# Kernel tuning notes

Hardware: AMD Instinct MI355X
Metric: run time of the kernel (lower is better)

The kernel has to match this reference:

```python
import jax, jax.numpy as jnp
import numpy as np

IMAGE_W = 256
IMAGE_H = 256
SIGMA = 0.2
EPS = 1e-07


def _gauss_filter(g, size, psize, pad):
    """g: [B,N] center coords in pixels. Returns [B,N,size,psize]."""
    # grid coords over padded canvas: value i - pad at row i (matches np.indices - pad)
    coords = jnp.arange(size + 2 * pad, dtype=jnp.float32) - pad          # [size+2pad]
    offs = jnp.arange(1, psize + 1, dtype=jnp.float32) - psize / 2 - 0.5  # [psize]
    mu = g[:, :, None] + offs[None, None, :]                              # [B,N,psize]
    F = jnp.exp(-(coords[None, None, :, None] - mu[:, :, None, :]) ** 2 / (2 * SIGMA ** 2))
    F = F / (F.sum(axis=2, keepdims=True) + EPS)
    return F[:, :, pad:size + pad]                                        # [B,N,size,psize]


def setup_inputs() -> dict:
    key = jax.random.key(0)
    k1, k2 = jax.random.split(key)
    brushes = jax.random.uniform(k1, (32, 64, 2), dtype=jnp.float32)
    patches = jax.random.normal(k2, (32, 64, 3, 16, 16), dtype=jnp.float32)
    return {"brushes": brushes, "patches": patches}


def reference(brushes, patches):
    B, N, C, ph, pw = patches.shape
    pad = ph // 2  # pad='half_patch'
    gx = brushes[:, :, 0] * IMAGE_W  # [B,N]
    gy = brushes[:, :, 1] * IMAGE_H
    Fx = _gauss_filter(gx, IMAGE_W, pw, pad)  # [B,N,w,pw]
    Fy = _gauss_filter(gy, IMAGE_H, ph, pad)  # [B,N,h,ph]
    # contract over pw: [B,N,C,w,ph]
    t = jnp.einsum('bnwq,bncpq->bncwp', Fx, patches)
    # contract over ph: [B,N,C,w,h]
    out = jnp.einsum('bncwp,bnhp->bncwh', t, Fy)
    out = out.mean(axis=1)            # [B,C,w,h]
    out = jnp.swapaxes(out, 2, 3)     # [B,C,h,w]
    return out
```

## Files before the change

### kernel.cpp

```cpp
#include <hip/hip_runtime.h>
#include <hip/hip_bf16.h>


#define E25 1.3887944e-11f

__global__ __launch_bounds__(256) void brush_tile32(
        const float* __restrict__ brushes,
        const float* __restrict__ patches,
        float* __restrict__ out)
{
    const int b    = blockIdx.z;
    const int tx   = blockIdx.x << 5;
    const int ty   = blockIdx.y << 5;
    const int tid  = threadIdx.x;
    const int lane = tid & 63;
    const int qi   = tid & 15;
    const int pi   = tid >> 4;

    __shared__ float4 T4[2 * 32 * 21];

    for (int i = tid; i < 320; i += 256) {
        const int buf = i / 160, r = i % 160;
        T4[buf * 672 + (r / 5) * 21 + 16 + (r % 5)] = make_float4(0, 0, 0, 0);
    }

    const float2 g0 = ((const float2*)brushes)[(b << 6) + lane];
    const float bx = g0.x * 256.0f, by = g0.y * 256.0f;
    const bool hit =
        (bx >= (float)tx - 9.5f) & (bx <= (float)tx + 40.5f) &
        (by >= (float)ty - 9.5f) & (by <= (float)ty + 40.5f);
    unsigned long long mask = __ballot(hit);

    float acc[2][2][3];
#pragma unroll
    for (int a = 0; a < 2; ++a)
#pragma unroll
        for (int h2 = 0; h2 < 2; ++h2)
            acc[a][h2][0] = acc[a][h2][1] = acc[a][h2][2] = 0.0f;

    int it = 0;
    while (mask) {
        const int n = __builtin_ctzll(mask);
        mask &= mask - 1;
        const float gx = __shfl(bx, n, 64);
        const float gy = __shfl(by, n, 64);
        const int buf = (it & 1) * 672; ++it;

        const float* pb = patches + (size_t)((b << 6) + n) * 768;
        const float r0 = pb[tid];
        const float r1 = pb[tid + 256];
        const float r2 = pb[tid + 512];

        float invz;
        {
            const int k = lane & 31;
            const float g  = (k >> 4) ? gy : gx;
            const float mu = g + (float)(k & 15) - 7.5f;
            const float fl = floorf(mu);
            float Z = 0.0f;
#pragma unroll
            for (int d = -1; d <= 2; ++d) {
                const float c = fl + (float)d;
                if (c >= -8.0f && c <= 263.0f) {
                    const float u = c - mu;
                    Z += __expf(-12.5f * u * u);
                }
            }
            invz = 1.0f / (Z + 1e-7f);
        }
        const float zx  = __shfl(invz, qi, 64);
        const float zyp = __shfl(invz, 16 + pi, 64);
        const float v0 = r0 * zx, v1 = r1 * zx, v2 = r2 * zx;

        const bool doA = (gx <= (float)tx + 24.5f);
        const bool doB = (gx >= (float)tx + 6.5f);

        float4 sA = make_float4(0, 0, 0, 0), sB = sA;
#pragma unroll
        for (int half = 0; half < 2; ++half) {
            const bool go = half ? doB : doA;
            if (!go) continue;
            const float ax = (float)(tx + (half << 4) + qi) - gx + 7.5f;
            const bool okx = (ax >= -2.5f) & (ax <= 17.5f);
            int qlo = (int)ceilf(ax - 2.0f);
            qlo = qlo < 0 ? 0 : (qlo > 15 ? 15 : qlo);
            float d0 = ax - (float)qlo;
            d0 = fminf(fmaxf(d0, -3.0f), 3.0f);
            float wgt = okx ? __expf(-12.5f * d0 * d0) : 0.0f;
            float u   = __expf(25.0f * d0 - 12.5f);
            const int base = ((pi & 3) << 4) + qlo;
            float4 s = make_float4(0, 0, 0, 0);
#pragma unroll
            for (int j = 0; j < 5; ++j) {
                const float a0 = __shfl(v0, base + j, 64);
                const float a1 = __shfl(v1, base + j, 64);
                const float a2 = __shfl(v2, base + j, 64);
                const float wj = (qlo + j < 16) ? wgt : 0.0f;
                s.x += wj * a0; s.y += wj * a1; s.z += wj * a2;
                wgt *= u; u *= E25;
            }
            s.x *= zyp; s.y *= zyp; s.z *= zyp;
            if (half) sB = s; else sA = s;
        }
        T4[buf + qi * 21 + pi]        = sA;
        T4[buf + (qi + 16) * 21 + pi] = sB;
        __syncthreads();

#pragma unroll
        for (int h2 = 0; h2 < 2; ++h2) {
            const float ay = (float)(ty + (h2 << 4) + pi) - gy + 7.5f;
            if (ay < -2.5f || ay > 17.5f) continue;
            int plo = (int)ceilf(ay - 2.0f);
            plo = plo < 0 ? 0 : (plo > 15 ? 15 : plo);
            const float d0 = ay - (float)plo;
            float wy[5];
            float wgt = __expf(-12.5f * d0 * d0);
            float u   = __expf(25.0f * d0 - 12.5f);
#pragma unroll
            for (int j = 0; j < 5; ++j) { wy[j] = wgt; wgt *= u; u *= E25; }
#pragma unroll
            for (int a = 0; a < 2; ++a) {
                if (!(a ? doB : doA)) continue;
                const float4* row = &T4[buf + (qi + (a << 4)) * 21 + plo];
                float s0 = 0.0f, s1 = 0.0f, s2 = 0.0f;
#pragma unroll
                for (int j = 0; j < 5; ++j) {
                    const float4 v = row[j];
                    s0 += wy[j] * v.x; s1 += wy[j] * v.y; s2 += wy[j] * v.z;
                }
                acc[a][h2][0] += s0; acc[a][h2][1] += s1; acc[a][h2][2] += s2;
            }
        }
    }

    const float sc = 1.0f / 64.0f;
#pragma unroll
    for (int a = 0; a < 2; ++a)
#pragma unroll
        for (int h2 = 0; h2 < 2; ++h2) {
            const int w = tx + (a << 4) + qi;
            const int h = ty + (h2 << 4) + pi;
            float* ob = out + (((size_t)(b * 3)) << 16) + (h << 8) + w;
            ob[0]       = acc[a][h2][0] * sc;
            ob[1 << 16] = acc[a][h2][1] * sc;
            ob[2 << 16] = acc[a][h2][2] * sc;
        }
}

extern "C" void kernel_launch(void* const* d_in, const int* in_sizes, int n_in,
                              void* d_out, int out_size, void* d_ws, size_t ws_size,
                              hipStream_t stream) {
    const float* brushes = (const float*)d_in[0];
    const float* patches = (const float*)d_in[1];
    float* out = (float*)d_out;
    brush_tile32<<<dim3(8, 8, 32), dim3(256), 0, stream>>>(brushes, patches, out);
}
```

Measured before the change: 80.64 us.

## Switch to one-wavefront blocks covering 16x16 output tiles

Replaces the 256-thread 32x32 tile kernel with a 64-thread kernel where one wavefront handles a 16x16 tile. Each lane processes four output rows and shuffles across four register groups. The smaller tile tightens the brush-overlap test so fewer brushes are visited per tile, and a single wave drops the cross-wave barrier cost and the double buffer. In exchange, patches are reloaded by more blocks and each lane does more shuffles.

```diff
diff --git a/kernel.cpp b/kernel.cpp
--- a/kernel.cpp
+++ b/kernel.cpp
@@ -4,58 +4,53 @@
 
 #define E25 1.3887944e-11f
 
-__global__ __launch_bounds__(256) void brush_tile32(
+__global__ __launch_bounds__(64) void brush_wave(
         const float* __restrict__ brushes,
         const float* __restrict__ patches,
         float* __restrict__ out)
 {
     const int b    = blockIdx.z;
-    const int tx   = blockIdx.x << 5;
-    const int ty   = blockIdx.y << 5;
-    const int tid  = threadIdx.x;
-    const int lane = tid & 63;
-    const int qi   = tid & 15;
-    const int pi   = tid >> 4;
+    const int tx   = blockIdx.x << 4;
+    const int ty   = blockIdx.y << 4;
+    const int lane = threadIdx.x;
+    const int qi   = lane & 15;
+    const int pi   = lane >> 4;
 
-    __shared__ float4 T4[2 * 32 * 21];
+    __shared__ float4 T4[16 * 21];
 
-    for (int i = tid; i < 320; i += 256) {
-        const int buf = i / 160, r = i % 160;
-        T4[buf * 672 + (r / 5) * 21 + 16 + (r % 5)] = make_float4(0, 0, 0, 0);
-    }
+    for (int i = lane; i < 80; i += 64)
+        T4[(i / 5) * 21 + 16 + (i % 5)] = make_float4(0, 0, 0, 0);
 
     const float2 g0 = ((const float2*)brushes)[(b << 6) + lane];
     const float bx = g0.x * 256.0f, by = g0.y * 256.0f;
     const bool hit =
-        (bx >= (float)tx - 9.5f) & (bx <= (float)tx + 40.5f) &
-        (by >= (float)ty - 9.5f) & (by <= (float)ty + 40.5f);
+        (bx >= (float)tx - 9.5f) & (bx <= (float)tx + 24.5f) &
+        (by >= (float)ty - 9.5f) & (by <= (float)ty + 24.5f);
     unsigned long long mask = __ballot(hit);
 
-    float acc[2][2][3];
+    float acc[4][3];
 #pragma unroll
-    for (int a = 0; a < 2; ++a)
-#pragma unroll
-        for (int h2 = 0; h2 < 2; ++h2)
-            acc[a][h2][0] = acc[a][h2][1] = acc[a][h2][2] = 0.0f;
+    for (int k = 0; k < 4; ++k) acc[k][0] = acc[k][1] = acc[k][2] = 0.0f;
 
-    int it = 0;
     while (mask) {
         const int n = __builtin_ctzll(mask);
         mask &= mask - 1;
         const float gx = __shfl(bx, n, 64);
         const float gy = __shfl(by, n, 64);
-        const int buf = (it & 1) * 672; ++it;
 
         const float* pb = patches + (size_t)((b << 6) + n) * 768;
-        const float r0 = pb[tid];
-        const float r1 = pb[tid + 256];
-        const float r2 = pb[tid + 512];
+        float r[3][4];
+#pragma unroll
+        for (int c = 0; c < 3; ++c)
+#pragma unroll
+            for (int k = 0; k < 4; ++k)
+                r[c][k] = pb[c * 256 + k * 64 + lane];
 
         float invz;
         {
-            const int k = lane & 31;
-            const float g  = (k >> 4) ? gy : gx;
-            const float mu = g + (float)(k & 15) - 7.5f;
+            const int k2 = lane & 31;
+            const float g  = (k2 >> 4) ? gy : gx;
+            const float mu = g + (float)(k2 & 15) - 7.5f;
             const float fl = floorf(mu);
             float Z = 0.0f;
 #pragma unroll
@@ -68,83 +63,75 @@
             }
             invz = 1.0f / (Z + 1e-7f);
         }
-        const float zx  = __shfl(invz, qi, 64);
-        const float zyp = __shfl(invz, 16 + pi, 64);
-        const float v0 = r0 * zx, v1 = r1 * zx, v2 = r2 * zx;
+        const float zx = __shfl(invz, qi, 64);
+        float zy[4];
+#pragma unroll
+        for (int k = 0; k < 4; ++k)
+            zy[k] = __shfl(invz, 16 + pi + 4 * k, 64);
 
-        const bool doA = (gx <= (float)tx + 24.5f);
-        const bool doB = (gx >= (float)tx + 6.5f);
+#pragma unroll
+        for (int c = 0; c < 3; ++c)
+#pragma unroll
+            for (int k = 0; k < 4; ++k)
+                r[c][k] *= zx;
 
-        float4 sA = make_float4(0, 0, 0, 0), sB = sA;
-#pragma unroll
-        for (int half = 0; half < 2; ++half) {
-            const bool go = half ? doB : doA;
-            if (!go) continue;
-            const float ax = (float)(tx + (half << 4) + qi) - gx + 7.5f;
-            const bool okx = (ax >= -2.5f) & (ax <= 17.5f);
+        {
+            const float ax  = (float)(tx + qi) - gx + 7.5f;
+            const bool  okx = (ax >= -2.5f) & (ax <= 17.5f);
             int qlo = (int)ceilf(ax - 2.0f);
             qlo = qlo < 0 ? 0 : (qlo > 15 ? 15 : qlo);
             float d0 = ax - (float)qlo;
             d0 = fminf(fmaxf(d0, -3.0f), 3.0f);
             float wgt = okx ? __expf(-12.5f * d0 * d0) : 0.0f;
             float u   = __expf(25.0f * d0 - 12.5f);
-            const int base = ((pi & 3) << 4) + qlo;
-            float4 s = make_float4(0, 0, 0, 0);
+            float s0[4] = {0, 0, 0, 0}, s1[4] = {0, 0, 0, 0}, s2[4] = {0, 0, 0, 0};
 #pragma unroll
             for (int j = 0; j < 5; ++j) {
-                const float a0 = __shfl(v0, base + j, 64);
-                const float a1 = __shfl(v1, base + j, 64);
-                const float a2 = __shfl(v2, base + j, 64);
-                const float wj = (qlo + j < 16) ? wgt : 0.0f;
-                s.x += wj * a0; s.y += wj * a1; s.z += wj * a2;
+                const float wj   = (qlo + j < 16) ? wgt : 0.0f;
+                const int   srcl = (pi << 4) + qlo + j;
+#pragma unroll
+                for (int k = 0; k < 4; ++k) {
+                    s0[k] += wj * __shfl(r[0][k], srcl, 64);
+                    s1[k] += wj * __shfl(r[1][k], srcl, 64);
+                    s2[k] += wj * __shfl(r[2][k], srcl, 64);
+                }
                 wgt *= u; u *= E25;
             }
-            s.x *= zyp; s.y *= zyp; s.z *= zyp;
-            if (half) sB = s; else sA = s;
+#pragma unroll
+            for (int k = 0; k < 4; ++k)
+                T4[qi * 21 + pi + 4 * k] =
+                    make_float4(s0[k] * zy[k], s1[k] * zy[k], s2[k] * zy[k], 0.0f);
         }
-        T4[buf + qi * 21 + pi]        = sA;
-        T4[buf + (qi + 16) * 21 + pi] = sB;
         __syncthreads();
 
 #pragma unroll
-        for (int h2 = 0; h2 < 2; ++h2) {
-            const float ay = (float)(ty + (h2 << 4) + pi) - gy + 7.5f;
+        for (int k = 0; k < 4; ++k) {
+            const float ay = (float)(ty + pi + 4 * k) - gy + 7.5f;
             if (ay < -2.5f || ay > 17.5f) continue;
             int plo = (int)ceilf(ay - 2.0f);
             plo = plo < 0 ? 0 : (plo > 15 ? 15 : plo);
             const float d0 = ay - (float)plo;
-            float wy[5];
             float wgt = __expf(-12.5f * d0 * d0);
             float u   = __expf(25.0f * d0 - 12.5f);
+            const float4* row = &T4[qi * 21 + plo];
 #pragma unroll
-            for (int j = 0; j < 5; ++j) { wy[j] = wgt; wgt *= u; u *= E25; }
-#pragma unroll
-            for (int a = 0; a < 2; ++a) {
-                if (!(a ? doB : doA)) continue;
-                const float4* row = &T4[buf + (qi + (a << 4)) * 21 + plo];
-                float s0 = 0.0f, s1 = 0.0f, s2 = 0.0f;
-#pragma unroll
-                for (int j = 0; j < 5; ++j) {
-                    const float4 v = row[j];
-                    s0 += wy[j] * v.x; s1 += wy[j] * v.y; s2 += wy[j] * v.z;
-                }
-                acc[a][h2][0] += s0; acc[a][h2][1] += s1; acc[a][h2][2] += s2;
+            for (int j = 0; j < 5; ++j) {
+                const float4 v = row[j];
+                acc[k][0] += wgt * v.x; acc[k][1] += wgt * v.y; acc[k][2] += wgt * v.z;
+                wgt *= u; u *= E25;
             }
         }
     }
 
     const float sc = 1.0f / 64.0f;
 #pragma unroll
-    for (int a = 0; a < 2; ++a)
-#pragma unroll
-        for (int h2 = 0; h2 < 2; ++h2) {
-            const int w = tx + (a << 4) + qi;
-            const int h = ty + (h2 << 4) + pi;
-            float* ob = out + (((size_t)(b * 3)) << 16) + (h << 8) + w;
-            ob[0]       = acc[a][h2][0] * sc;
-            ob[1 << 16] = acc[a][h2][1] * sc;
-            ob[2 << 16] = acc[a][h2][2] * sc;
-        }
+    for (int k = 0; k < 4; ++k) {
+        const int h = ty + pi + 4 * k;
+        float* ob = out + (((size_t)(b * 3)) << 16) + (h << 8) + tx + qi;
+        ob[0]       = acc[k][0] * sc;
+        ob[1 << 16] = acc[k][1] * sc;
+        ob[2 << 16] = acc[k][2] * sc;
+    }
 }
 
 extern "C" void kernel_launch(void* const* d_in, const int* in_sizes, int n_in,
@@ -153,5 +140,5 @@
     const float* brushes = (const float*)d_in[0];
     const float* patches = (const float*)d_in[1];
     float* out = (float*)d_out;
-    brush_tile32<<<dim3(8, 8, 32), dim3(256), 0, stream>>>(brushes, patches, out);
+    brush_wave<<<dim3(16, 16, 32), dim3(64), 0, stream>>>(brushes, patches, out);
 }
```

Result: no change. 81.76 us (+1.4%).
